# Performance work log

Measured on AMD Instinct MI355X. Metric: run time of the kernel, lower is better.

Reference implementation:

```python
import jax, jax.numpy as jnp
from jax import lax
import numpy as np

EPS = 1e-3  # keras BatchNormalization default epsilon

def _bn(x, g, b, m, v):
    return (x - m) / jnp.sqrt(v + EPS) * g + b

def _conv_relu(x, w, b):
    y = lax.conv_general_dilated(x, w, (1, 1), 'SAME', dimension_numbers=('NHWC', 'HWIO', 'NHWC'))
    return jax.nn.relu(y + b)

def _pool(x):
    return lax.reduce_window(x, -jnp.inf, lax.max, (1, 2, 2, 1), (1, 2, 2, 1), 'VALID')

def setup_inputs():
    key = jax.random.key(0)
    ks = jax.random.split(key, 24)
    B, E = 2048, 16
    rn = lambda k, s, sc=0.05: jax.random.normal(k, s, jnp.float32) * sc
    pos = lambda k, s: jax.random.uniform(k, s, jnp.float32, 0.5, 1.5)
    inp = {}
    inp['x'] = jax.random.normal(ks[0], (B, 32, 32, 3), jnp.float32)
    inp['cW1'] = rn(ks[1], (3, 3, 3, 32), 0.2); inp['cb1'] = jnp.zeros((32,), jnp.float32)
    inp['bn1g'] = pos(ks[2], (32,)); inp['bn1b'] = rn(ks[3], (32,))
    inp['bn1m'] = rn(ks[4], (32,)); inp['bn1v'] = pos(ks[5], (32,))
    inp['cW2'] = rn(ks[6], (3, 3, 32, 64), 0.1); inp['cb2'] = jnp.zeros((64,), jnp.float32)
    inp['bn2g'] = pos(ks[7], (64,)); inp['bn2b'] = rn(ks[8], (64,))
    inp['bn2m'] = rn(ks[9], (64,)); inp['bn2v'] = pos(ks[10], (64,))
    inp['dW'] = rn(ks[11], (4096, 128), 0.02); inp['db'] = jnp.zeros((128,), jnp.float32)
    inp['rW1'] = rn(ks[12], (128, 64), 0.1); inp['rb1'] = jnp.zeros((64,), jnp.float32)
    inp['rW2'] = rn(ks[13], (64, E), 0.1); inp['rb2'] = jnp.zeros((E,), jnp.float32)
    inp['eW1'] = rn(ks[14], (E, 128, 128), 0.1); inp['eb1'] = jnp.zeros((E, 128), jnp.float32)
    inp['ebng'] = pos(ks[15], (E, 128)); inp['ebnb'] = rn(ks[16], (E, 128))
    inp['ebnm'] = rn(ks[17], (E, 128)); inp['ebnv'] = pos(ks[18], (E, 128))
    inp['eW2'] = rn(ks[19], (E, 128, 64), 0.1); inp['eb2'] = jnp.zeros((E, 64), jnp.float32)
    inp['eW3'] = rn(ks[20], (E, 64, 10), 0.1); inp['eb3'] = jnp.zeros((E, 10), jnp.float32)
    return inp

def reference(x, cW1, cb1, bn1g, bn1b, bn1m, bn1v, cW2, cb2, bn2g, bn2b, bn2m, bn2v,
              dW, db, rW1, rb1, rW2, rb2, eW1, eb1, ebng, ebnb, ebnm, ebnv, eW2, eb2, eW3, eb3):
    # shared trunk: conv(relu) -> BN -> maxpool, twice; flatten; dense(relu). Dropout = identity (inference).
    h = _pool(_bn(_conv_relu(x, cW1, cb1), bn1g, bn1b, bn1m, bn1v))   # [B,16,16,32]
    h = _pool(_bn(_conv_relu(h, cW2, cb2), bn2g, bn2b, bn2m, bn2v))   # [B,8,8,64]
    feats = jax.nn.relu(h.reshape(h.shape[0], -1) @ dW + db)          # [B,128]
    # router softmax over expert logits
    router_logits = jax.nn.relu(feats @ rW1 + rb1) @ rW2 + rb2        # [B,E]
    router_probs = jax.nn.softmax(router_logits, axis=-1)
    # all experts fused into batched GEMMs over stacked weights: [E,B,*]
    e = jax.nn.relu(jnp.einsum('bd,edh->ebh', feats, eW1) + eb1[:, None, :])
    e = _bn(e, ebng[:, None, :], ebnb[:, None, :], ebnm[:, None, :], ebnv[:, None, :])
    e = jax.nn.relu(jnp.einsum('ebh,ehk->ebk', e, eW2) + eb2[:, None, :])
    e = jnp.einsum('ebk,ekc->ebc', e, eW3) + eb3[:, None, :]          # [E,B,10]
    # weighted sum combine: sum_e probs[b,e] * logits[e,b,c]
    return jnp.einsum('ebc,be->bc', e, router_probs)
```

## Files before the change

kernel.cpp:

```cpp
#include <hip/hip_runtime.h>

#define EPS 1e-3f

typedef _Float16 half8 __attribute__((ext_vector_type(8)));
typedef _Float16 half4v __attribute__((ext_vector_type(4)));
typedef float f32x4 __attribute__((ext_vector_type(4)));

__global__ __launch_bounds__(256) void k_wprep_all(
    const float* __restrict__ dW,  _Float16* __restrict__ Wt2,
    const float* __restrict__ eW1, _Float16* __restrict__ eW1t,
    const float* __restrict__ eW2, _Float16* __restrict__ eW2t,
    const float* __restrict__ cW1, _Float16* __restrict__ Wt1,
    const float* __restrict__ cW2, _Float16* __restrict__ Wt,
    const float* __restrict__ eW3, _Float16* __restrict__ eW3p)
{
    __shared__ _Float16 lsbuf[16640];
    int bx = blockIdx.x, tid = threadIdx.x;

    if (bx < 64) {
        auto lt = (_Float16(*)[137])lsbuf;
        int kb = bx * 64;
        int c = tid & 127, r2 = tid >> 7;
#pragma unroll
        for (int it = 0; it < 32; ++it) {
            int r = it * 2 + r2;
            lt[r][c] = (_Float16)dW[(long)(kb + r) * 128 + c];
        }
        __syncthreads();
#pragma unroll
        for (int it = 0; it < 4; ++it) {
            int chunk = it * 256 + tid;
            int n = chunk >> 3, kc = (chunk & 7) * 8;
            half8 v;
#pragma unroll
            for (int j = 0; j < 8; ++j) v[j] = lt[kc + j][n];
            *(half8*)(Wt2 + (long)n * 4096 + kb + kc) = v;
        }
    } else if (bx < 80) {
        auto lt = (_Float16(*)[130])lsbuf;
        int e = bx - 64;
        const float* src = eW1 + (long)e * 16384;
#pragma unroll
        for (int it = 0; it < 64; ++it) {
            int idx = it * 256 + tid;
            lt[idx >> 7][idx & 127] = (_Float16)src[idx];
        }
        __syncthreads();
        _Float16* dst = eW1t + (long)e * 16384;
#pragma unroll
        for (int it = 0; it < 64; ++it) {
            int idx = it * 256 + tid;
            dst[idx] = lt[idx & 127][idx >> 7];
        }
    } else if (bx < 96) {
        auto lt = (_Float16(*)[66])lsbuf;
        int e = bx - 80;
        const float* src = eW2 + (long)e * 8192;
#pragma unroll
        for (int it = 0; it < 32; ++it) {
            int idx = it * 256 + tid;
            lt[idx >> 6][idx & 63] = (_Float16)src[idx];
        }
        __syncthreads();
        _Float16* dst = eW2t + (long)e * 8192;
#pragma unroll
        for (int it = 0; it < 32; ++it) {
            int idx = it * 256 + tid;
            dst[idx] = lt[idx & 127][idx >> 7];
        }
    } else {
        int t = (bx - 96) * 256 + tid;
        if (t < 2048) {
            int k = t & 31, co = (t >> 5) & 31, p = t >> 10;
            int kyin = (k >> 4) & 1, kxp = (k >> 2) & 3, ci = k & 3;
            int ky = 2 * p + kyin;
            float val = (ky < 3 && kxp < 3 && ci < 3)
                        ? cW1[((ky * 3 + kxp) * 3 + ci) * 32 + co] : 0.f;
            Wt1[t] = (_Float16)val;
        } else if (t >= 3072 && t < 3072 + 18432) {
            int u = t - 3072;
            int co = u & 63;
            int rest = u >> 6;
            int ci = rest & 31, tap = rest >> 5;
            Wt[(tap * 64 + co) * 32 + ci] = (_Float16)cW2[u];
        } else if (t >= 21504 && t < 21504 + 16384) {
            int u = t - 21504;
            int k = u & 63, n = (u >> 6) & 15, e = u >> 10;
            float val = (n < 10) ? eW3[(e * 64 + k) * 10 + n] : 0.f;
            eW3p[(e * 16 + n) * 64 + k] = (_Float16)val;
        }
    }
}

__global__ __launch_bounds__(256) void k_conv12(
    const float* __restrict__ x, const _Float16* __restrict__ Wt1,
    const float* __restrict__ b1, const float* __restrict__ g1,
    const float* __restrict__ bb1, const float* __restrict__ m1,
    const float* __restrict__ v1,
    const _Float16* __restrict__ Wt,
    const float* __restrict__ b2, const float* __restrict__ g2,
    const float* __restrict__ bb2, const float* __restrict__ m2,
    const float* __restrict__ v2,
    _Float16* __restrict__ out)
{
    __shared__ __align__(16) _Float16 As1[35][40][4];
    __shared__ __align__(16) _Float16 As2[18][18][40];
    int tid = threadIdx.x;
    int b = blockIdx.x;
    int w = tid >> 6, l = tid & 63;
    int l15 = l & 15, lq = l >> 4;
    int lqr = lq >> 1, lqc = (lq & 1) * 2;

    {
        half4v z4 = { (_Float16)0.f, (_Float16)0.f, (_Float16)0.f, (_Float16)0.f };
        for (int i = tid; i < 216; i += 256) {
            int row, col;
            if (i < 120) { int rr = i / 40; row = (rr == 0) ? 0 : 32 + rr; col = i % 40; }
            else         { int j = i - 120; row = 1 + j / 3; int cc = j % 3; col = (cc == 0) ? 0 : 32 + cc; }
            *(half4v*)&As1[row][col][0] = z4;
        }
        float4 z = make_float4(0.f, 0.f, 0.f, 0.f);
        for (int i = tid; i < 272; i += 256) {
            int pair = i >> 2, q = i & 3;
            int row, col;
            if      (pair < 18) { row = 0;  col = pair; }
            else if (pair < 36) { row = 17; col = pair - 18; }
            else if (pair < 52) { row = pair - 36 + 1; col = 0; }
            else                { row = pair - 52 + 1; col = 17; }
            *(float4*)&As2[row][col][q * 8] = z;
        }
    }

    {
        int y = tid >> 3, x0 = (tid & 7) * 4;
        const float* src = x + ((long)b * 1024 + y * 32 + x0) * 3;
        float4 f0 = *(const float4*)(src);
        float4 f1 = *(const float4*)(src + 4);
        float4 f2 = *(const float4*)(src + 8);
        half4v h0 = { (_Float16)f0.x, (_Float16)f0.y, (_Float16)f0.z, (_Float16)0.f };
        half4v h1 = { (_Float16)f0.w, (_Float16)f1.x, (_Float16)f1.y, (_Float16)0.f };
        half4v h2 = { (_Float16)f1.z, (_Float16)f1.w, (_Float16)f2.x, (_Float16)0.f };
        half4v h3 = { (_Float16)f2.y, (_Float16)f2.z, (_Float16)f2.w, (_Float16)0.f };
        *(half4v*)&As1[y + 1][x0 + 1][0] = h0;
        *(half4v*)&As1[y + 1][x0 + 2][0] = h1;
        *(half4v*)&As1[y + 1][x0 + 3][0] = h2;
        *(half4v*)&As1[y + 1][x0 + 4][0] = h3;
    }

    half8 bf1[2][2];
#pragma unroll
    for (int p = 0; p < 2; ++p)
#pragma unroll
        for (int nf = 0; nf < 2; ++nf)
            bf1[p][nf] = *(const half8*)(Wt1 + (p * 32 + nf * 16 + l15) * 32 + lq * 8);

    float bv1[2], S1[2], T1[2];
#pragma unroll
    for (int nf = 0; nf < 2; ++nf) {
        int co = nf * 16 + l15;
        bv1[nf] = b1[co];
        float s = rsqrtf(v1[co] + EPS) * g1[co];
        S1[nf] = s;
        T1[nf] = bb1[co] - m1[co] * s;
    }
    __syncthreads();

    {
        int y0 = w * 8;
#pragma unroll
        for (int pr = 0; pr < 4; ++pr) {
            int ya = y0 + 2 * pr;
            f32x4 acc[2][2][2];
#pragma unroll
            for (int r = 0; r < 2; ++r)
#pragma unroll
                for (int h = 0; h < 2; ++h)
#pragma unroll
                    for (int nf = 0; nf < 2; ++nf)
                        acc[r][h][nf] = (f32x4){ bv1[nf], bv1[nf], bv1[nf], bv1[nf] };

#pragma unroll
            for (int p = 0; p < 2; ++p)
#pragma unroll
                for (int r = 0; r < 2; ++r)
#pragma unroll
                    for (int h = 0; h < 2; ++h) {
                        const _Float16* ap = &As1[ya + r + 2 * p + lqr][h * 16 + l15 + lqc][0];
                        half4v a0 = *(const half4v*)ap;
                        half4v a1 = *(const half4v*)(ap + 4);
                        half8 af = __builtin_shufflevector(a0, a1, 0, 1, 2, 3, 4, 5, 6, 7);
#pragma unroll
                        for (int nf = 0; nf < 2; ++nf)
                            acc[r][h][nf] = __builtin_amdgcn_mfma_f32_16x16x32_f16(
                                af, bf1[p][nf], acc[r][h][nf], 0, 0, 0);
                    }

            int py = w * 4 + pr;
#pragma unroll
            for (int h = 0; h < 2; ++h)
#pragma unroll
                for (int nf = 0; nf < 2; ++nf) {
                    f32x4 aA = acc[0][h][nf], aB = acc[1][h][nf];
                    float p0 = fmaxf(fmaxf(aA[0], aA[1]), fmaxf(aB[0], aB[1]));
                    float p1 = fmaxf(fmaxf(aA[2], aA[3]), fmaxf(aB[2], aB[3]));
                    p0 = fmaxf(p0, 0.f); p1 = fmaxf(p1, 0.f);
                    p0 = fmaf(p0, S1[nf], T1[nf]);
                    p1 = fmaf(p1, S1[nf], T1[nf]);
                    int px = h * 8 + lq * 2;
                    int co = nf * 16 + l15;
                    As2[py + 1][px + 1][co] = (_Float16)p0;
                    As2[py + 1][px + 2][co] = (_Float16)p1;
                }
        }
    }
    __syncthreads();

    f32x4 acc2[4][4];
#pragma unroll
    for (int nf = 0; nf < 4; ++nf) {
        float bv = b2[nf * 16 + l15];
#pragma unroll
        for (int mf = 0; mf < 4; ++mf)
            acc2[mf][nf] = (f32x4){ bv, bv, bv, bv };
    }

    int row0 = 4 * w;
#pragma unroll
    for (int tap = 0; tap < 9; ++tap) {
        int ky = tap / 3, kx = tap % 3;
        half8 bf[4];
        const _Float16* wb = Wt + ((long)(tap * 64 + l15)) * 32 + lq * 8;
#pragma unroll
        for (int nf = 0; nf < 4; ++nf)
            bf[nf] = *(const half8*)(wb + (long)nf * 16 * 32);
#pragma unroll
        for (int mf = 0; mf < 4; ++mf) {
            const _Float16* ap = &As2[row0 + mf + ky][l15 + kx][lq * 8];
            half8 af = *(const half8*)ap;
#pragma unroll
            for (int nf = 0; nf < 4; ++nf)
                acc2[mf][nf] = __builtin_amdgcn_mfma_f32_16x16x32_f16(
                    af, bf[nf], acc2[mf][nf], 0, 0, 0);
        }
    }

#pragma unroll
    for (int nf = 0; nf < 4; ++nf) {
        int co = nf * 16 + l15;
        float s = rsqrtf(v2[co] + EPS) * g2[co];
        float t2 = bb2[co] - m2[co] * s;
#pragma unroll
        for (int pr = 0; pr < 2; ++pr) {
            int prow = 2 * w + pr;
            f32x4 a0 = acc2[2 * pr][nf];
            f32x4 a1 = acc2[2 * pr + 1][nf];
            float p0 = fmaxf(fmaxf(a0[0], a0[1]), fmaxf(a1[0], a1[1]));
            float p1 = fmaxf(fmaxf(a0[2], a0[3]), fmaxf(a1[2], a1[3]));
            p0 = fmaxf(p0, 0.f);
            p1 = fmaxf(p1, 0.f);
            int ppx = lq * 2;
            long base = (((long)b * 8 + prow) * 8) * 64 + co;
            out[base + (long)(ppx    ) * 64] = (_Float16)fmaf(p0, s, t2);
            out[base + (long)(ppx + 1) * 64] = (_Float16)fmaf(p1, s, t2);
        }
    }
}

__global__ __launch_bounds__(256) void k_dense_mfma(
    const _Float16* __restrict__ h2f, const _Float16* __restrict__ Wt2,
    _Float16* __restrict__ pws)
{
    __shared__ __align__(16) _Float16 As[16][264];
    int tid = threadIdx.x;
    int w = tid >> 6, l = tid & 63;
    int l15 = l & 15, lq = l >> 4;
    int brow = blockIdx.x * 16;
    int kbase = blockIdx.y * 512;
    int n0 = w * 32;

    f32x4 acc[2] = { (f32x4){0.f,0.f,0.f,0.f}, (f32x4){0.f,0.f,0.f,0.f} };

    int srow = tid >> 4, sc = (tid & 15) * 16;
#pragma unroll
    for (int k0 = 0; k0 < 512; k0 += 256) {
        __syncthreads();
        const _Float16* src = h2f + (long)(brow + srow) * 4096 + kbase + k0 + sc;
        half8 v0 = *(const half8*)src;
        half8 v1 = *(const half8*)(src + 8);
        *(half8*)(&As[srow][sc])     = v0;
        *(half8*)(&As[srow][sc + 8]) = v1;
        __syncthreads();
#pragma unroll
        for (int kk = 0; kk < 256; kk += 32) {
            half8 af = *(const half8*)(&As[l15][kk + lq * 8]);
#pragma unroll
            for (int nf = 0; nf < 2; ++nf) {
                half8 bf = *(const half8*)(Wt2 + (long)(n0 + nf * 16 + l15) * 4096
                                           + kbase + k0 + kk + lq * 8);
                acc[nf] = __builtin_amdgcn_mfma_f32_16x16x32_f16(af, bf, acc[nf], 0, 0, 0);
            }
        }
    }

    _Float16* pbase = pws + (long)blockIdx.y * 262144;
#pragma unroll
    for (int nf = 0; nf < 2; ++nf) {
        int n = n0 + nf * 16 + l15;
#pragma unroll
        for (int reg = 0; reg < 4; ++reg) {
            int b = brow + lq * 4 + reg;
            pbase[(long)b * 128 + n] = (_Float16)acc[nf][reg];
        }
    }
}

__global__ __launch_bounds__(256) void k_reduce_router(
    const _Float16* __restrict__ pws, const float* __restrict__ db,
    const float* __restrict__ rW1, const float* __restrict__ rb1,
    const float* __restrict__ rW2, const float* __restrict__ rb2,
    _Float16* __restrict__ featsH, float* __restrict__ probs)
{
    __shared__ float fsm[8][128];
    __shared__ float r1s[8][64];
    int tid = threadIdx.x;
    int brow = blockIdx.x * 8;
    int r = tid >> 5, c0 = (tid & 31) * 4;

    float acc[4];
#pragma unroll
    for (int j = 0; j < 4; ++j) acc[j] = db[c0 + j];
    long base = (long)(brow + r) * 128 + c0;
#pragma unroll
    for (int kc = 0; kc < 8; ++kc) {
        half4v v0 = *(const half4v*)(pws + (long)kc * 262144 + base);
#pragma unroll
        for (int j = 0; j < 4; ++j) acc[j] += (float)v0[j];
    }
    half4v hv;
#pragma unroll
    for (int j = 0; j < 4; ++j) {
        float val = fmaxf(acc[j], 0.f);
        fsm[r][c0 + j] = val;
        hv[j] = (_Float16)val;
    }
    *(half4v*)(featsH + base) = hv;
    __syncthreads();

    {
        int h = tid & 63, bg = tid >> 6;
        float a[2];
#pragma unroll
        for (int i = 0; i < 2; ++i) a[i] = rb1[h];
        for (int d = 0; d < 128; ++d) {
            float wgt = rW1[d * 64 + h];
#pragma unroll
            for (int i = 0; i < 2; ++i) a[i] += fsm[bg * 2 + i][d] * wgt;
        }
#pragma unroll
        for (int i = 0; i < 2; ++i) r1s[bg * 2 + i][h] = fmaxf(a[i], 0.f);
    }
    __syncthreads();

    if (tid < 128) {
        int b = tid >> 4, e = tid & 15;
        float a = rb2[e];
#pragma unroll 8
        for (int k = 0; k < 64; ++k) a += r1s[b][k] * rW2[k * 16 + e];
        float mx = a;
#pragma unroll
        for (int off = 1; off < 16; off <<= 1)
            mx = fmaxf(mx, __shfl_xor(mx, off, 16));
        float ex = __expf(a - mx);
        float s = ex;
#pragma unroll
        for (int off = 1; off < 16; off <<= 1)
            s += __shfl_xor(s, off, 16);
        probs[(long)(brow + b) * 16 + e] = ex / s;
    }
}

__global__ __launch_bounds__(512) void k_expert_mfma(
    const _Float16* __restrict__ featsH,
    const _Float16* __restrict__ eW1t, const float* __restrict__ eb1,
    const float* __restrict__ g,  const float* __restrict__ bb,
    const float* __restrict__ m,  const float* __restrict__ v,
    const _Float16* __restrict__ eW2t, const float* __restrict__ eb2,
    const _Float16* __restrict__ eW3p, const float* __restrict__ eb3,
    float* __restrict__ e3p)
{
    __shared__ __align__(16) _Float16 fsH[64][136];
    __shared__ __align__(16) _Float16 h1sH[64][136];
    __shared__ __align__(16) _Float16 h2sH[64][72];
    int e = blockIdx.x, bt = blockIdx.y;
    int tid = threadIdx.x;
    int w = tid >> 6, l = tid & 63, l15 = l & 15, lq = l >> 4;
    int brow = bt * 64;
    int m0 = (w & 3) * 16;
    int nh = w >> 2;

#pragma unroll
    for (int it = 0; it < 2; ++it) {
        int idx = it * 512 + tid;
        int r = idx >> 4, c = (idx & 15) * 8;
        *(half8*)&fsH[r][c] = *(const half8*)(featsH + (long)(brow + r) * 128 + c);
    }
    __syncthreads();

    {
        half8 af[4];
#pragma unroll
        for (int kq = 0; kq < 4; ++kq)
            af[kq] = *(const half8*)&fsH[m0 + l15][kq * 32 + lq * 8];
        const _Float16* B1 = eW1t + (long)e * 16384 + (long)nh * 8192 + l15 * 128 + lq * 8;
        f32x4 acc[4];
#pragma unroll
        for (int nf = 0; nf < 4; ++nf) {
            float bv = eb1[e * 128 + nh * 64 + nf * 16 + l15];
            acc[nf] = (f32x4){ bv, bv, bv, bv };
        }
#pragma unroll
        for (int nf = 0; nf < 4; ++nf)
#pragma unroll
            for (int kq = 0; kq < 4; ++kq) {
                half8 bfv = *(const half8*)(B1 + nf * 2048 + kq * 32);
                acc[nf] = __builtin_amdgcn_mfma_f32_16x16x32_f16(af[kq], bfv, acc[nf], 0, 0, 0);
            }
#pragma unroll
        for (int nf = 0; nf < 4; ++nf) {
            int h = nh * 64 + nf * 16 + l15;
            float gg = g[e * 128 + h], bbv = bb[e * 128 + h], mm = m[e * 128 + h];
            float iv = rsqrtf(v[e * 128 + h] + EPS);
#pragma unroll
            for (int reg = 0; reg < 4; ++reg) {
                float val = fmaxf(acc[nf][reg], 0.f);
                h1sH[m0 + lq * 4 + reg][h] = (_Float16)((val - mm) * iv * gg + bbv);
            }
        }
    }
    __syncthreads();

    {
        half8 af[4];
#pragma unroll
        for (int kq = 0; kq < 4; ++kq)
            af[kq] = *(const half8*)&h1sH[m0 + l15][kq * 32 + lq * 8];
        const _Float16* B2 = eW2t + (long)e * 8192 + (long)nh * 4096 + l15 * 128 + lq * 8;
        f32x4 acc[2];
#pragma unroll
        for (int nf = 0; nf < 2; ++nf) {
            float bv = eb2[e * 64 + nh * 32 + nf * 16 + l15];
            acc[nf] = (f32x4){ bv, bv, bv, bv };
        }
#pragma unroll
        for (int nf = 0; nf < 2; ++nf)
#pragma unroll
            for (int kq = 0; kq < 4; ++kq) {
                half8 bfv = *(const half8*)(B2 + nf * 2048 + kq * 32);
                acc[nf] = __builtin_amdgcn_mfma_f32_16x16x32_f16(af[kq], bfv, acc[nf], 0, 0, 0);
            }
#pragma unroll
        for (int nf = 0; nf < 2; ++nf)
#pragma unroll
            for (int reg = 0; reg < 4; ++reg)
                h2sH[m0 + lq * 4 + reg][nh * 32 + nf * 16 + l15] =
                    (_Float16)fmaxf(acc[nf][reg], 0.f);
    }
    __syncthreads();

    if (nh == 0) {
        half8 af[2];
#pragma unroll
        for (int kq = 0; kq < 2; ++kq)
            af[kq] = *(const half8*)&h2sH[m0 + l15][kq * 32 + lq * 8];
        const _Float16* B3 = eW3p + (long)e * 1024 + l15 * 64 + lq * 8;
        float bv = (l15 < 10) ? eb3[e * 10 + l15] : 0.f;
        f32x4 acc = (f32x4){ bv, bv, bv, bv };
#pragma unroll
        for (int kq = 0; kq < 2; ++kq) {
            half8 bfv = *(const half8*)(B3 + kq * 32);
            acc = __builtin_amdgcn_mfma_f32_16x16x32_f16(af[kq], bfv, acc, 0, 0, 0);
        }
#pragma unroll
        for (int reg = 0; reg < 4; ++reg) {
            int b = brow + m0 + lq * 4 + reg;
            e3p[((long)e * 2048 + b) * 16 + l15] = acc[reg];
        }
    }
}

__global__ __launch_bounds__(256) void k_combine(
    const float* __restrict__ e3p, const float* __restrict__ probs,
    float* __restrict__ out)
{
    int t = blockIdx.x * blockDim.x + threadIdx.x;
    if (t >= 2048 * 10) return;
    int b = t / 10, c = t % 10;
    float acc = 0.f;
#pragma unroll
    for (int e = 0; e < 16; ++e)
        acc += probs[(long)b * 16 + e] * e3p[((long)e * 2048 + b) * 16 + c];
    out[t] = acc;
}

extern "C" void kernel_launch(void* const* d_in, const int* in_sizes, int n_in,
                              void* d_out, int out_size, void* d_ws, size_t ws_size,
                              hipStream_t stream)
{
    const float* x    = (const float*)d_in[0];
    const float* cW1  = (const float*)d_in[1];
    const float* cb1  = (const float*)d_in[2];
    const float* bn1g = (const float*)d_in[3];
    const float* bn1b = (const float*)d_in[4];
    const float* bn1m = (const float*)d_in[5];
    const float* bn1v = (const float*)d_in[6];
    const float* cW2  = (const float*)d_in[7];
    const float* cb2  = (const float*)d_in[8];
    const float* bn2g = (const float*)d_in[9];
    const float* bn2b = (const float*)d_in[10];
    const float* bn2m = (const float*)d_in[11];
    const float* bn2v = (const float*)d_in[12];
    const float* dW   = (const float*)d_in[13];
    const float* db   = (const float*)d_in[14];
    const float* rW1  = (const float*)d_in[15];
    const float* rb1  = (const float*)d_in[16];
    const float* rW2  = (const float*)d_in[17];
    const float* rb2  = (const float*)d_in[18];
    const float* eW1  = (const float*)d_in[19];
    const float* eb1  = (const float*)d_in[20];
    const float* ebng = (const float*)d_in[21];
    const float* ebnb = (const float*)d_in[22];
    const float* ebnm = (const float*)d_in[23];
    const float* ebnv = (const float*)d_in[24];
    const float* eW2  = (const float*)d_in[25];
    const float* eb2  = (const float*)d_in[26];
    const float* eW3  = (const float*)d_in[27];
    const float* eb3  = (const float*)d_in[28];

    float* ws    = (float*)d_ws;
    float* h1reg = ws;
    float* e3p   = h1reg;
    _Float16* featsH = (_Float16*)(h1reg + 524288);
    float* h2reg = h1reg + 16777216;
    _Float16* h2f = (_Float16*)h2reg;
    _Float16* Wt2 = (_Float16*)(h2reg + 4194304);
    float* probs = h2reg + 8388608;
    float* ewreg = probs + 32768;
    _Float16* eW1t = (_Float16*)ewreg;
    _Float16* eW2t = eW1t + 262144;
    _Float16* eW3p = eW2t + 131072;
    _Float16* Wt   = eW3p + 16384;
    _Float16* Wt1  = Wt + 18432;
    _Float16* pws = (_Float16*)(ewreg + 262144);
    float* out   = (float*)d_out;

    k_wprep_all<<<244, 256, 0, stream>>>(dW, Wt2, eW1, eW1t, eW2, eW2t,
                                         cW1, Wt1, cW2, Wt, eW3, eW3p);
    k_conv12<<<2048, 256, 0, stream>>>(x, Wt1, cb1, bn1g, bn1b, bn1m, bn1v,
                                       Wt, cb2, bn2g, bn2b, bn2m, bn2v, h2f);
    {
        dim3 grid(128, 8);
        k_dense_mfma<<<grid, 256, 0, stream>>>(h2f, Wt2, pws);
    }
    k_reduce_router<<<256, 256, 0, stream>>>(pws, db, rW1, rb1, rW2, rb2,
                                             featsH, probs);
    {
        dim3 grid(16, 32);
        k_expert_mfma<<<grid, 512, 0, stream>>>(featsH, eW1t, eb1, ebng, ebnb, ebnm, ebnv,
                                                eW2t, eb2, eW3p, eb3, e3p);
    }
    k_combine<<<80, 256, 0, stream>>>(e3p, probs, out);
}
```

Before: 86.53 us.

## Process two images per conv block and prefetch second image during conv2

```diff
diff --git a/kernel.cpp b/kernel.cpp
--- a/kernel.cpp
+++ b/kernel.cpp
@@ -92,6 +92,111 @@
     }
 }
 
+__device__ __forceinline__ void conv12_phaseA(
+    _Float16 (*As1)[40][4], _Float16 (*As2)[18][40],
+    const half8 bf1[2][2], const float bv1[2], const float S1[2], const float T1[2],
+    int w, int l15, int lq, int lqr, int lqc)
+{
+    int y0 = w * 8;
+#pragma unroll
+    for (int pr = 0; pr < 4; ++pr) {
+        int ya = y0 + 2 * pr;
+        f32x4 acc[2][2][2];
+#pragma unroll
+        for (int r = 0; r < 2; ++r)
+#pragma unroll
+            for (int h = 0; h < 2; ++h)
+#pragma unroll
+                for (int nf = 0; nf < 2; ++nf)
+                    acc[r][h][nf] = (f32x4){ bv1[nf], bv1[nf], bv1[nf], bv1[nf] };
+
+#pragma unroll
+        for (int p = 0; p < 2; ++p)
+#pragma unroll
+            for (int r = 0; r < 2; ++r)
+#pragma unroll
+                for (int h = 0; h < 2; ++h) {
+                    const _Float16* ap = &As1[ya + r + 2 * p + lqr][h * 16 + l15 + lqc][0];
+                    half4v a0 = *(const half4v*)ap;
+                    half4v a1 = *(const half4v*)(ap + 4);
+                    half8 af = __builtin_shufflevector(a0, a1, 0, 1, 2, 3, 4, 5, 6, 7);
+#pragma unroll
+                    for (int nf = 0; nf < 2; ++nf)
+                        acc[r][h][nf] = __builtin_amdgcn_mfma_f32_16x16x32_f16(
+                            af, bf1[p][nf], acc[r][h][nf], 0, 0, 0);
+                }
+
+        int py = w * 4 + pr;
+#pragma unroll
+        for (int h = 0; h < 2; ++h)
+#pragma unroll
+            for (int nf = 0; nf < 2; ++nf) {
+                f32x4 aA = acc[0][h][nf], aB = acc[1][h][nf];
+                float p0 = fmaxf(fmaxf(aA[0], aA[1]), fmaxf(aB[0], aB[1]));
+                float p1 = fmaxf(fmaxf(aA[2], aA[3]), fmaxf(aB[2], aB[3]));
+                p0 = fmaxf(p0, 0.f); p1 = fmaxf(p1, 0.f);
+                p0 = fmaf(p0, S1[nf], T1[nf]);
+                p1 = fmaf(p1, S1[nf], T1[nf]);
+                int px = h * 8 + lq * 2;
+                int co = nf * 16 + l15;
+                As2[py + 1][px + 1][co] = (_Float16)p0;
+                As2[py + 1][px + 2][co] = (_Float16)p1;
+            }
+    }
+}
+
+__device__ __forceinline__ void conv12_phaseB(
+    _Float16 (*As2)[18][40], const _Float16* __restrict__ Wt,
+    const float bv2[4], const float S2[4], const float T2[4],
+    _Float16* __restrict__ out, long b, int w, int l15, int lq)
+{
+    f32x4 acc2[4][4];
+#pragma unroll
+    for (int nf = 0; nf < 4; ++nf)
+#pragma unroll
+        for (int mf = 0; mf < 4; ++mf)
+            acc2[mf][nf] = (f32x4){ bv2[nf], bv2[nf], bv2[nf], bv2[nf] };
+
+    int row0 = 4 * w;
+#pragma unroll
+    for (int tap = 0; tap < 9; ++tap) {
+        int ky = tap / 3, kx = tap % 3;
+        half8 bf[4];
+        const _Float16* wb = Wt + ((long)(tap * 64 + l15)) * 32 + lq * 8;
+#pragma unroll
+        for (int nf = 0; nf < 4; ++nf)
+            bf[nf] = *(const half8*)(wb + (long)nf * 16 * 32);
+#pragma unroll
+        for (int mf = 0; mf < 4; ++mf) {
+            const _Float16* ap = &As2[row0 + mf + ky][l15 + kx][lq * 8];
+            half8 af = *(const half8*)ap;
+#pragma unroll
+            for (int nf = 0; nf < 4; ++nf)
+                acc2[mf][nf] = __builtin_amdgcn_mfma_f32_16x16x32_f16(
+                    af, bf[nf], acc2[mf][nf], 0, 0, 0);
+        }
+    }
+
+#pragma unroll
+    for (int nf = 0; nf < 4; ++nf) {
+        int co = nf * 16 + l15;
+#pragma unroll
+        for (int pr = 0; pr < 2; ++pr) {
+            int prow = 2 * w + pr;
+            f32x4 a0 = acc2[2 * pr][nf];
+            f32x4 a1 = acc2[2 * pr + 1][nf];
+            float p0 = fmaxf(fmaxf(a0[0], a0[1]), fmaxf(a1[0], a1[1]));
+            float p1 = fmaxf(fmaxf(a0[2], a0[3]), fmaxf(a1[2], a1[3]));
+            p0 = fmaxf(p0, 0.f);
+            p1 = fmaxf(p1, 0.f);
+            int ppx = lq * 2;
+            long base = ((b * 8 + prow) * 8) * 64 + co;
+            out[base + (long)(ppx    ) * 64] = (_Float16)fmaf(p0, S2[nf], T2[nf]);
+            out[base + (long)(ppx + 1) * 64] = (_Float16)fmaf(p1, S2[nf], T2[nf]);
+        }
+    }
+}
+
 __global__ __launch_bounds__(256) void k_conv12(
     const float* __restrict__ x, const _Float16* __restrict__ Wt1,
     const float* __restrict__ b1, const float* __restrict__ g1,
@@ -106,7 +211,7 @@
     __shared__ __align__(16) _Float16 As1[35][40][4];
     __shared__ __align__(16) _Float16 As2[18][18][40];
     int tid = threadIdx.x;
-    int b = blockIdx.x;
+    long img0 = (long)blockIdx.x * 2, img1 = img0 + 1;
     int w = tid >> 6, l = tid & 63;
     int l15 = l & 15, lq = l >> 4;
     int lqr = lq >> 1, lqc = (lq & 1) * 2;
@@ -131,9 +236,10 @@
         }
     }
 
-    {
-        int y = tid >> 3, x0 = (tid & 7) * 4;
-        const float* src = x + ((long)b * 1024 + y * 32 + x0) * 3;
+    int sy = tid >> 3, sx0 = (tid & 7) * 4;
+
+    {
+        const float* src = x + (img0 * 1024 + sy * 32 + sx0) * 3;
         float4 f0 = *(const float4*)(src);
         float4 f1 = *(const float4*)(src + 4);
         float4 f2 = *(const float4*)(src + 8);
@@ -141,10 +247,10 @@
         half4v h1 = { (_Float16)f0.w, (_Float16)f1.x, (_Float16)f1.y, (_Float16)0.f };
         half4v h2 = { (_Float16)f1.z, (_Float16)f1.w, (_Float16)f2.x, (_Float16)0.f };
         half4v h3 = { (_Float16)f2.y, (_Float16)f2.z, (_Float16)f2.w, (_Float16)0.f };
-        *(half4v*)&As1[y + 1][x0 + 1][0] = h0;
-        *(half4v*)&As1[y + 1][x0 + 2][0] = h1;
-        *(half4v*)&As1[y + 1][x0 + 3][0] = h2;
-        *(half4v*)&As1[y + 1][x0 + 4][0] = h3;
+        *(half4v*)&As1[sy + 1][sx0 + 1][0] = h0;
+        *(half4v*)&As1[sy + 1][sx0 + 2][0] = h1;
+        *(half4v*)&As1[sy + 1][sx0 + 3][0] = h2;
+        *(half4v*)&As1[sy + 1][sx0 + 4][0] = h3;
     }
 
     half8 bf1[2][2];
@@ -163,107 +269,44 @@
         S1[nf] = s;
         T1[nf] = bb1[co] - m1[co] * s;
     }
-    __syncthreads();
-
-    {
-        int y0 = w * 8;
-#pragma unroll
-        for (int pr = 0; pr < 4; ++pr) {
-            int ya = y0 + 2 * pr;
-            f32x4 acc[2][2][2];
-#pragma unroll
-            for (int r = 0; r < 2; ++r)
-#pragma unroll
-                for (int h = 0; h < 2; ++h)
-#pragma unroll
-                    for (int nf = 0; nf < 2; ++nf)
-                        acc[r][h][nf] = (f32x4){ bv1[nf], bv1[nf], bv1[nf], bv1[nf] };
-
-#pragma unroll
-            for (int p = 0; p < 2; ++p)
-#pragma unroll
-                for (int r = 0; r < 2; ++r)
-#pragma unroll
-                    for (int h = 0; h < 2; ++h) {
-                        const _Float16* ap = &As1[ya + r + 2 * p + lqr][h * 16 + l15 + lqc][0];
-                        half4v a0 = *(const half4v*)ap;
-                        half4v a1 = *(const half4v*)(ap + 4);
-                        half8 af = __builtin_shufflevector(a0, a1, 0, 1, 2, 3, 4, 5, 6, 7);
-#pragma unroll
-                        for (int nf = 0; nf < 2; ++nf)
-                            acc[r][h][nf] = __builtin_amdgcn_mfma_f32_16x16x32_f16(
-                                af, bf1[p][nf], acc[r][h][nf], 0, 0, 0);
-                    }
-
-            int py = w * 4 + pr;
-#pragma unroll
-            for (int h = 0; h < 2; ++h)
-#pragma unroll
-                for (int nf = 0; nf < 2; ++nf) {
-                    f32x4 aA = acc[0][h][nf], aB = acc[1][h][nf];
-                    float p0 = fmaxf(fmaxf(aA[0], aA[1]), fmaxf(aB[0], aB[1]));
-                    float p1 = fmaxf(fmaxf(aA[2], aA[3]), fmaxf(aB[2], aB[3]));
-                    p0 = fmaxf(p0, 0.f); p1 = fmaxf(p1, 0.f);
-                    p0 = fmaf(p0, S1[nf], T1[nf]);
-                    p1 = fmaf(p1, S1[nf], T1[nf]);
-                    int px = h * 8 + lq * 2;
-                    int co = nf * 16 + l15;
-                    As2[py + 1][px + 1][co] = (_Float16)p0;
-                    As2[py + 1][px + 2][co] = (_Float16)p1;
-                }
-        }
-    }
-    __syncthreads();
-
-    f32x4 acc2[4][4];
-#pragma unroll
-    for (int nf = 0; nf < 4; ++nf) {
-        float bv = b2[nf * 16 + l15];
-#pragma unroll
-        for (int mf = 0; mf < 4; ++mf)
-            acc2[mf][nf] = (f32x4){ bv, bv, bv, bv };
-    }
-
-    int row0 = 4 * w;
-#pragma unroll
-    for (int tap = 0; tap < 9; ++tap) {
-        int ky = tap / 3, kx = tap % 3;
-        half8 bf[4];
-        const _Float16* wb = Wt + ((long)(tap * 64 + l15)) * 32 + lq * 8;
-#pragma unroll
-        for (int nf = 0; nf < 4; ++nf)
-            bf[nf] = *(const half8*)(wb + (long)nf * 16 * 32);
-#pragma unroll
-        for (int mf = 0; mf < 4; ++mf) {
-            const _Float16* ap = &As2[row0 + mf + ky][l15 + kx][lq * 8];
-            half8 af = *(const half8*)ap;
-#pragma unroll
-            for (int nf = 0; nf < 4; ++nf)
-                acc2[mf][nf] = __builtin_amdgcn_mfma_f32_16x16x32_f16(
-                    af, bf[nf], acc2[mf][nf], 0, 0, 0);
-        }
-    }
-
+    float bv2[4], S2[4], T2[4];
 #pragma unroll
     for (int nf = 0; nf < 4; ++nf) {
         int co = nf * 16 + l15;
+        bv2[nf] = b2[co];
         float s = rsqrtf(v2[co] + EPS) * g2[co];
-        float t2 = bb2[co] - m2[co] * s;
-#pragma unroll
-        for (int pr = 0; pr < 2; ++pr) {
-            int prow = 2 * w + pr;
-            f32x4 a0 = acc2[2 * pr][nf];
-            f32x4 a1 = acc2[2 * pr + 1][nf];
-            float p0 = fmaxf(fmaxf(a0[0], a0[1]), fmaxf(a1[0], a1[1]));
-            float p1 = fmaxf(fmaxf(a0[2], a0[3]), fmaxf(a1[2], a1[3]));
-            p0 = fmaxf(p0, 0.f);
-            p1 = fmaxf(p1, 0.f);
-            int ppx = lq * 2;
-            long base = (((long)b * 8 + prow) * 8) * 64 + co;
-            out[base + (long)(ppx    ) * 64] = (_Float16)fmaf(p0, s, t2);
-            out[base + (long)(ppx + 1) * 64] = (_Float16)fmaf(p1, s, t2);
-        }
-    }
+        S2[nf] = s;
+        T2[nf] = bb2[co] - m2[co] * s;
+    }
+    __syncthreads();
+
+    conv12_phaseA(As1, As2, bf1, bv1, S1, T1, w, l15, lq, lqr, lqc);
+    __syncthreads();
+
+    float4 g0, g1v, g2v;
+    {
+        const float* src = x + (img1 * 1024 + sy * 32 + sx0) * 3;
+        g0  = *(const float4*)(src);
+        g1v = *(const float4*)(src + 4);
+        g2v = *(const float4*)(src + 8);
+    }
+    conv12_phaseB(As2, Wt, bv2, S2, T2, out, img0, w, l15, lq);
+    {
+        half4v h0 = { (_Float16)g0.x,  (_Float16)g0.y,  (_Float16)g0.z,  (_Float16)0.f };
+        half4v h1 = { (_Float16)g0.w,  (_Float16)g1v.x, (_Float16)g1v.y, (_Float16)0.f };
+        half4v h2 = { (_Float16)g1v.z, (_Float16)g1v.w, (_Float16)g2v.x, (_Float16)0.f };
+        half4v h3 = { (_Float16)g2v.y, (_Float16)g2v.z, (_Float16)g2v.w, (_Float16)0.f };
+        *(half4v*)&As1[sy + 1][sx0 + 1][0] = h0;
+        *(half4v*)&As1[sy + 1][sx0 + 2][0] = h1;
+        *(half4v*)&As1[sy + 1][sx0 + 3][0] = h2;
+        *(half4v*)&As1[sy + 1][sx0 + 4][0] = h3;
+    }
+    __syncthreads();
+
+    conv12_phaseA(As1, As2, bf1, bv1, S1, T1, w, l15, lq, lqr, lqc);
+    __syncthreads();
+
+    conv12_phaseB(As2, Wt, bv2, S2, T2, out, img1, w, l15, lq);
 }
 
 __global__ __launch_bounds__(256) void k_dense_mfma(
@@ -555,7 +598,7 @@
 
     k_wprep_all<<<244, 256, 0, stream>>>(dW, Wt2, eW1, eW1t, eW2, eW2t,
                                          cW1, Wt1, cW2, Wt, eW3, eW3p);
-    k_conv12<<<2048, 256, 0, stream>>>(x, Wt1, cb1, bn1g, bn1b, bn1m, bn1v,
+    k_conv12<<<1024, 256, 0, stream>>>(x, Wt1, cb1, bn1g, bn1b, bn1m, bn1v,
                                        Wt, cb2, bn2g, bn2b, bn2m, bn2v, h2f);
     {
         dim3 grid(128, 8);
```

New measurement: 85.09 us, median of 2. Within noise of the previous version (-1.7%).
